# Optimization experiments

Measured on AMD Instinct MI355X. Metric: run time of the kernel, lower is better.

## Reference

```python
import jax, jax.numpy as jnp
import numpy as np

LAYER_SIZES = [3, 3, 3]
CHANNELS = 192
BATCH = 65536
FULL_SIZES = [1] + LAYER_SIZES + [1]  # 1 -> 3 -> 3 -> 3 -> 1
NUM_LAYERS = len(LAYER_SIZES) + 1     # 4


def setup_inputs() -> dict:
    key = jax.random.key(0)
    ks = jax.random.split(key, 1 + len(LAYER_SIZES) + NUM_LAYERS + NUM_LAYERS)
    inp = {"x": jax.random.normal(ks[0], (BATCH, CHANNELS, 1), dtype=jnp.float32)}
    i = 1
    for k, sz in enumerate(LAYER_SIZES):
        inp[f"a{k}"] = jax.random.normal(ks[i], (CHANNELS, sz), dtype=jnp.float32); i += 1
    for k in range(NUM_LAYERS):  # b[k] has size full_sizes[k+1]
        inp[f"b{k}"] = jax.random.normal(ks[i], (CHANNELS, FULL_SIZES[k + 1]), dtype=jnp.float32); i += 1
    for k in range(NUM_LAYERS):
        inp[f"H{k}"] = jax.random.normal(ks[i], (CHANNELS, FULL_SIZES[k], FULL_SIZES[k + 1]), dtype=jnp.float32); i += 1
    return inp


def _cdf(x, a_list, b_list, H_list):
    # x: (B, C, 1)
    for k in range(NUM_LAYERS - 1):
        # per-channel matmul: (B,C,M) x (C,M,P) -> (B,C,P), with softplus-constrained H
        x = jnp.einsum('bni,nip->bnp', x, jax.nn.softplus(H_list[k])) + b_list[k]
        x = x + jnp.tanh(a_list[k]) * jnp.tanh(x)
    x = jnp.einsum('bni,nip->bnp', x, jax.nn.softplus(H_list[-1])) + b_list[-1]
    return jax.nn.sigmoid(x)


def reference(x, a0, a1, a2, b0, b1, b2, b3, H0, H1, H2, H3):
    a_list = [a0, a1, a2]
    b_list = [b0, b1, b2, b3]
    H_list = [H0, H1, H2, H3]
    # PDF of y_tilde: c(x + 1/2) - c(x - 1/2)
    half = jnp.asarray(0.5, dtype=x.dtype)
    p = _cdf(x + half, a_list, b_list, H_list) - _cdf(x - half, a_list, b_list, H_list)
    return p
```

## Files before the change

### kernel.cpp

```cpp
#include <hip/hip_runtime.h>
#include <hip/hip_bf16.h>
#include <math.h>

#define CHN 192
#define BATCHN 65536
#define NBLOCKS 4096
#define ROWS_PER_BLOCK (BATCHN / NBLOCKS)
#define NWS 61

#define KSCALE 2.885390081777926f
#define LOG2E  1.4426950408889634f

__device__ __forceinline__ float fast_rcp(float x)  { return __builtin_amdgcn_rcpf(x); }
__device__ __forceinline__ float fast_exp2(float x) { return __builtin_amdgcn_exp2f(x); }
__device__ __forceinline__ void pinf(float& v) { asm volatile("" : "+v"(v)); }

__device__ __forceinline__ float softplus_acc(float h) {
    if (h > 20.0f) return h;
    return log1pf(expf(h));
}

__global__ __launch_bounds__(CHN) void weights_kernel(
    const float* __restrict__ a0, const float* __restrict__ a1, const float* __restrict__ a2,
    const float* __restrict__ b0, const float* __restrict__ b1, const float* __restrict__ b2,
    const float* __restrict__ b3,
    const float* __restrict__ H0, const float* __restrict__ H1, const float* __restrict__ H2,
    const float* __restrict__ H3,
    float* __restrict__ ws)
{
    const int c = threadIdx.x;
#pragma unroll
    for (int i = 0; i < 3; ++i) {
        float w0k = KSCALE * softplus_acc(H0[c * 3 + i]);
        float h   = 0.5f * w0k;
        float t1k0 = KSCALE * tanhf(a0[c * 3 + i]);
        ws[(0  + i) * CHN + c] = w0k;
        ws[(3  + i) * CHN + c] = KSCALE * b0[c * 3 + i];
        ws[(6  + i) * CHN + c] = exp2f(h);
        ws[(9  + i) * CHN + c] = exp2f(-h);
        ws[(12 + i) * CHN + c] = h + t1k0;
        ws[(15 + i) * CHN + c] = -h + t1k0;
        ws[(18 + i) * CHN + c] = -2.0f * t1k0;

        float t1k1 = KSCALE * tanhf(a1[c * 3 + i]);
        ws[(30 + i) * CHN + c] = KSCALE * b1[c * 3 + i];
        ws[(33 + i) * CHN + c] = t1k1;
        ws[(36 + i) * CHN + c] = -2.0f * t1k1;

        float t1k2 = KSCALE * tanhf(a2[c * 3 + i]);
        ws[(48 + i) * CHN + c] = KSCALE * b2[c * 3 + i];
        ws[(51 + i) * CHN + c] = t1k2;
        ws[(54 + i) * CHN + c] = -2.0f * t1k2;

        ws[(57 + i) * CHN + c] = -0.5f * softplus_acc(H3[c * 3 + i]);
    }
#pragma unroll
    for (int i = 0; i < 9; ++i) {
        ws[(21 + i) * CHN + c] = softplus_acc(H1[c * 9 + i]);
        ws[(39 + i) * CHN + c] = softplus_acc(H2[c * 9 + i]);
    }
    ws[60 * CHN + c] = -LOG2E * b3[c];
}

__device__ __forceinline__ float density_pair(const float* __restrict__ W, float xv) {
    float vp[3], vm[3];
#pragma unroll
    for (int i = 0; i < 3; ++i) {
        float q  = fmaf(W[0 + i], xv, W[3 + i]);
        float E  = fast_exp2(q);
        float rp = fast_rcp(fmaf(E, W[6 + i], 1.0f));
        float rm = fast_rcp(fmaf(E, W[9 + i], 1.0f));
        vp[i] = fmaf(W[18 + i], rp, q + W[12 + i]);
        vm[i] = fmaf(W[18 + i], rm, q + W[15 + i]);
    }
    float zp[3], zm[3];
#pragma unroll
    for (int p = 0; p < 3; ++p) {
        float tp = W[30 + p], tm = W[30 + p];
#pragma unroll
        for (int i = 0; i < 3; ++i) {
            tp = fmaf(vp[i], W[21 + i * 3 + p], tp);
            tm = fmaf(vm[i], W[21 + i * 3 + p], tm);
        }
        float rp = fast_rcp(fast_exp2(tp) + 1.0f);
        float rm = fast_rcp(fast_exp2(tm) + 1.0f);
        zp[p] = fmaf(W[36 + p], rp, tp + W[33 + p]);
        zm[p] = fmaf(W[36 + p], rm, tm + W[33 + p]);
    }
    float yp[3], ym[3];
#pragma unroll
    for (int p = 0; p < 3; ++p) {
        float tp = W[48 + p], tm = W[48 + p];
#pragma unroll
        for (int i = 0; i < 3; ++i) {
            tp = fmaf(zp[i], W[39 + i * 3 + p], tp);
            tm = fmaf(zm[i], W[39 + i * 3 + p], tm);
        }
        float rp = fast_rcp(fast_exp2(tp) + 1.0f);
        float rm = fast_rcp(fast_exp2(tm) + 1.0f);
        yp[p] = fmaf(W[54 + p], rp, tp + W[51 + p]);
        ym[p] = fmaf(W[54 + p], rm, tm + W[51 + p]);
    }
    float sp = W[60], sm = W[60];
#pragma unroll
    for (int i = 0; i < 3; ++i) {
        sp = fmaf(yp[i], W[57 + i], sp);
        sm = fmaf(ym[i], W[57 + i], sm);
    }
    float pp = fast_rcp(fast_exp2(sp) + 1.0f);
    float pm = fast_rcp(fast_exp2(sm) + 1.0f);
    return pp - pm;
}

__global__ __launch_bounds__(CHN, 1) void density_kernel(
    const float* __restrict__ x,
    const float* __restrict__ wt,
    float* __restrict__ out)
{
    const int c = threadIdx.x;

    float W[NWS];
#pragma unroll
    for (int s = 0; s < NWS; ++s) W[s] = wt[s * CHN + c];
#pragma unroll
    for (int s = 0; s < NWS; ++s) pinf(W[s]);

    const int b_start = blockIdx.x * ROWS_PER_BLOCK;
#pragma unroll 2
    for (int r = 0; r < ROWS_PER_BLOCK; ++r) {
        const int idx = (b_start + r) * CHN + c;
        out[idx] = density_pair(W, x[idx]);
    }
}

extern "C" void kernel_launch(void* const* d_in, const int* in_sizes, int n_in,
                              void* d_out, int out_size, void* d_ws, size_t ws_size,
                              hipStream_t stream) {
    const float* x  = (const float*)d_in[0];
    const float* a0 = (const float*)d_in[1];
    const float* a1 = (const float*)d_in[2];
    const float* a2 = (const float*)d_in[3];
    const float* b0 = (const float*)d_in[4];
    const float* b1 = (const float*)d_in[5];
    const float* b2 = (const float*)d_in[6];
    const float* b3 = (const float*)d_in[7];
    const float* H0 = (const float*)d_in[8];
    const float* H1 = (const float*)d_in[9];
    const float* H2 = (const float*)d_in[10];
    const float* H3 = (const float*)d_in[11];
    float* out = (float*)d_out;
    float* ws  = (float*)d_ws;

    weights_kernel<<<1, CHN, 0, stream>>>(a0, a1, a2, b0, b1, b2, b3,
                                          H0, H1, H2, H3, ws);
    density_kernel<<<NBLOCKS, CHN, 0, stream>>>(x, ws, out);
}
```

Measured before the change: 82.09 us.

## Stage per-channel weights in LDS and process row slabs per thread

```diff
diff --git a/kernel.cpp b/kernel.cpp
--- a/kernel.cpp
+++ b/kernel.cpp
@@ -4,16 +4,19 @@
 
 #define CHN 192
 #define BATCHN 65536
-#define NBLOCKS 4096
-#define ROWS_PER_BLOCK (BATCHN / NBLOCKS)
 #define NWS 61
+#define BLOCKT 384
+#define ROWS_PER_BLOCK 64
+#define ROWS_PER_GROUP 32
+#define RSLAB 4
+#define NSLABS (ROWS_PER_GROUP / RSLAB)
+#define NBLOCKS (BATCHN / ROWS_PER_BLOCK)
 
 #define KSCALE 2.885390081777926f
 #define LOG2E  1.4426950408889634f
 
 __device__ __forceinline__ float fast_rcp(float x)  { return __builtin_amdgcn_rcpf(x); }
 __device__ __forceinline__ float fast_exp2(float x) { return __builtin_amdgcn_exp2f(x); }
-__device__ __forceinline__ void pinf(float& v) { asm volatile("" : "+v"(v)); }
 
 __device__ __forceinline__ float softplus_acc(float h) {
     if (h > 20.0f) return h;
@@ -62,74 +65,94 @@
     ws[60 * CHN + c] = -LOG2E * b3[c];
 }
 
-__device__ __forceinline__ float density_pair(const float* __restrict__ W, float xv) {
-    float vp[3], vm[3];
-#pragma unroll
-    for (int i = 0; i < 3; ++i) {
-        float q  = fmaf(W[0 + i], xv, W[3 + i]);
-        float E  = fast_exp2(q);
-        float rp = fast_rcp(fmaf(E, W[6 + i], 1.0f));
-        float rm = fast_rcp(fmaf(E, W[9 + i], 1.0f));
-        vp[i] = fmaf(W[18 + i], rp, q + W[12 + i]);
-        vm[i] = fmaf(W[18 + i], rm, q + W[15 + i]);
-    }
-    float zp[3], zm[3];
-#pragma unroll
-    for (int p = 0; p < 3; ++p) {
-        float tp = W[30 + p], tm = W[30 + p];
-#pragma unroll
-        for (int i = 0; i < 3; ++i) {
-            tp = fmaf(vp[i], W[21 + i * 3 + p], tp);
-            tm = fmaf(vm[i], W[21 + i * 3 + p], tm);
-        }
-        float rp = fast_rcp(fast_exp2(tp) + 1.0f);
-        float rm = fast_rcp(fast_exp2(tm) + 1.0f);
-        zp[p] = fmaf(W[36 + p], rp, tp + W[33 + p]);
-        zm[p] = fmaf(W[36 + p], rm, tm + W[33 + p]);
-    }
-    float yp[3], ym[3];
-#pragma unroll
-    for (int p = 0; p < 3; ++p) {
-        float tp = W[48 + p], tm = W[48 + p];
-#pragma unroll
-        for (int i = 0; i < 3; ++i) {
-            tp = fmaf(zp[i], W[39 + i * 3 + p], tp);
-            tm = fmaf(zm[i], W[39 + i * 3 + p], tm);
-        }
-        float rp = fast_rcp(fast_exp2(tp) + 1.0f);
-        float rm = fast_rcp(fast_exp2(tm) + 1.0f);
-        yp[p] = fmaf(W[54 + p], rp, tp + W[51 + p]);
-        ym[p] = fmaf(W[54 + p], rm, tm + W[51 + p]);
-    }
-    float sp = W[60], sm = W[60];
-#pragma unroll
-    for (int i = 0; i < 3; ++i) {
-        sp = fmaf(yp[i], W[57 + i], sp);
-        sm = fmaf(ym[i], W[57 + i], sm);
-    }
-    float pp = fast_rcp(fast_exp2(sp) + 1.0f);
-    float pm = fast_rcp(fast_exp2(sm) + 1.0f);
-    return pp - pm;
-}
-
-__global__ __launch_bounds__(CHN, 1) void density_kernel(
+__global__ __launch_bounds__(BLOCKT, 4) void density_kernel(
     const float* __restrict__ x,
     const float* __restrict__ wt,
     float* __restrict__ out)
 {
-    const int c = threadIdx.x;
+    __shared__ float4 sW4[(NWS * CHN) / 4];
+    float* sW = reinterpret_cast<float*>(sW4);
 
-    float W[NWS];
+    const int tid = threadIdx.x;
+
+    const float4* w4 = reinterpret_cast<const float4*>(wt);
+    constexpr int NV = (NWS * CHN) / 4;
+    for (int j = tid; j < NV; j += BLOCKT) sW4[j] = w4[j];
+    __syncthreads();
+
+    const int c = tid % CHN;
+    const int g = tid / CHN;
+    const int row0 = blockIdx.x * ROWS_PER_BLOCK + g * ROWS_PER_GROUP;
+
+    for (int sl = 0; sl < NSLABS; ++sl) {
+        int off = 0;
+        asm volatile("" : "+v"(off));
+        const float* Wl = sW + c + off;
+#define WS(s) Wl[(s) * CHN]
+
+        const int base = (row0 + sl * RSLAB) * CHN + c;
+        float xv[RSLAB];
 #pragma unroll
-    for (int s = 0; s < NWS; ++s) W[s] = wt[s * CHN + c];
+        for (int r = 0; r < RSLAB; ++r) xv[r] = x[base + r * CHN];
+
+        float vp[RSLAB][3], vm[RSLAB][3];
 #pragma unroll
-    for (int s = 0; s < NWS; ++s) pinf(W[s]);
-
-    const int b_start = blockIdx.x * ROWS_PER_BLOCK;
-#pragma unroll 2
-    for (int r = 0; r < ROWS_PER_BLOCK; ++r) {
-        const int idx = (b_start + r) * CHN + c;
-        out[idx] = density_pair(W, x[idx]);
+        for (int i = 0; i < 3; ++i) {
+            float w0k = WS(0 + i),  b0k = WS(3 + i);
+            float cp  = WS(6 + i),  cm  = WS(9 + i);
+            float gp  = WS(12 + i), gm  = WS(15 + i), t2 = WS(18 + i);
+#pragma unroll
+            for (int r = 0; r < RSLAB; ++r) {
+                float q  = fmaf(w0k, xv[r], b0k);
+                float E  = fast_exp2(q);
+                float rp = fast_rcp(fmaf(E, cp, 1.0f));
+                float rm = fast_rcp(fmaf(E, cm, 1.0f));
+                vp[r][i] = fmaf(t2, rp, q + gp);
+                vm[r][i] = fmaf(t2, rm, q + gm);
+            }
+        }
+        float zp[RSLAB][3], zm[RSLAB][3];
+#pragma unroll
+        for (int p = 0; p < 3; ++p) {
+            float w0 = WS(21 + p), w1 = WS(24 + p), w2 = WS(27 + p);
+            float bb = WS(30 + p), t1 = WS(33 + p), t2 = WS(36 + p);
+#pragma unroll
+            for (int r = 0; r < RSLAB; ++r) {
+                float tp = fmaf(vp[r][2], w2, fmaf(vp[r][1], w1, fmaf(vp[r][0], w0, bb)));
+                float tm = fmaf(vm[r][2], w2, fmaf(vm[r][1], w1, fmaf(vm[r][0], w0, bb)));
+                float rp = fast_rcp(fast_exp2(tp) + 1.0f);
+                float rm = fast_rcp(fast_exp2(tm) + 1.0f);
+                zp[r][p] = fmaf(t2, rp, tp + t1);
+                zm[r][p] = fmaf(t2, rm, tm + t1);
+            }
+        }
+        float yp[RSLAB][3], ym[RSLAB][3];
+#pragma unroll
+        for (int p = 0; p < 3; ++p) {
+            float w0 = WS(39 + p), w1 = WS(42 + p), w2 = WS(45 + p);
+            float bb = WS(48 + p), t1 = WS(51 + p), t2 = WS(54 + p);
+#pragma unroll
+            for (int r = 0; r < RSLAB; ++r) {
+                float tp = fmaf(zp[r][2], w2, fmaf(zp[r][1], w1, fmaf(zp[r][0], w0, bb)));
+                float tm = fmaf(zm[r][2], w2, fmaf(zm[r][1], w1, fmaf(zm[r][0], w0, bb)));
+                float rp = fast_rcp(fast_exp2(tp) + 1.0f);
+                float rm = fast_rcp(fast_exp2(tm) + 1.0f);
+                yp[r][p] = fmaf(t2, rp, tp + t1);
+                ym[r][p] = fmaf(t2, rm, tm + t1);
+            }
+        }
+        {
+            float w30 = WS(57), w31 = WS(58), w32 = WS(59), b3n = WS(60);
+#pragma unroll
+            for (int r = 0; r < RSLAB; ++r) {
+                float sp = fmaf(yp[r][2], w32, fmaf(yp[r][1], w31, fmaf(yp[r][0], w30, b3n)));
+                float sm = fmaf(ym[r][2], w32, fmaf(ym[r][1], w31, fmaf(ym[r][0], w30, b3n)));
+                float pp = fast_rcp(fast_exp2(sp) + 1.0f);
+                float pm = fast_rcp(fast_exp2(sm) + 1.0f);
+                out[base + r * CHN] = pp - pm;
+            }
+        }
+#undef WS
     }
 }
 
@@ -153,5 +176,5 @@
 
     weights_kernel<<<1, CHN, 0, stream>>>(a0, a1, a2, b0, b1, b2, b3,
                                           H0, H1, H2, H3, ws);
-    density_kernel<<<NBLOCKS, CHN, 0, stream>>>(x, ws, out);
+    density_kernel<<<NBLOCKS, BLOCKT, 0, stream>>>(x, ws, out);
 }
```

After: 99.19 us. 1.21x slower.
